# Kernel tuning notes

Hardware: AMD Instinct MI355X
Metric: run time of the kernel (lower is better)

Reference implementation:

```python
import jax, jax.numpy as jnp
from jax import lax
import numpy as np

CHANNEL_N = 16
EMB = 128
B, H, W = 16, 256, 256


def setup_inputs() -> dict:
    key = jax.random.key(0)
    ks = jax.random.split(key, 8)
    x = jax.random.uniform(ks[0], (B, CHANNEL_N, H, W), dtype=jnp.float32)
    fire_mask = (jax.random.uniform(ks[1], (B, 1, H, W)) < 0.5).astype(jnp.float32)
    s = 0.05
    w1 = jax.random.normal(ks[2], (3 * CHANNEL_N, EMB), dtype=jnp.float32) * s
    b1 = jnp.zeros((EMB,), jnp.float32)
    w2 = jax.random.normal(ks[3], (EMB, EMB), dtype=jnp.float32) * s
    b2 = jnp.zeros((EMB,), jnp.float32)
    w3 = jax.random.normal(ks[4], (EMB, CHANNEL_N), dtype=jnp.float32) * s
    b3 = jnp.zeros((CHANNEL_N,), jnp.float32)
    return {"x": x, "fire_mask": fire_mask, "w1": w1, "b1": b1, "w2": w2, "b2": b2, "w3": w3, "b3": b3}


def _forward(x, fire_mask, w1, b1, w2, b2, w3, b3):
    # depthwise Sobel conv (torch conv2d = cross-correlation, same as lax default)
    sob = jnp.array([[-1., 0., 1.], [-2., 0., 2.], [-1., 0., 1.]], jnp.float32)
    kx = jnp.tile(sob[None, None], (CHANNEL_N, 1, 1, 1))   # OIHW, groups=16
    ky = jnp.tile(sob.T[None, None], (CHANNEL_N, 1, 1, 1))
    conv = lambda k: lax.conv_general_dilated(x, k, (1, 1), 'SAME', feature_group_count=CHANNEL_N)
    feats = jnp.concatenate([x, conv(kx), conv(ky)], axis=1)  # [B,48,H,W]

    # alive mask: 3x3 max-pool of alpha channel > 0.1
    alpha = x[:, 3:4]
    pooled = lax.reduce_window(alpha, -jnp.inf, lax.max, (1, 1, 3, 3), (1, 1, 1, 1), 'SAME')
    alive = (pooled > 0.1).astype(x.dtype)
    combined = fire_mask * alive                     # [B,1,H,W]
    # nonzero-indexing semantics: update written wherever combined != 0
    sel = (combined != 0).astype(x.dtype)

    f = feats.transpose(0, 2, 3, 1)                  # [B,H,W,48]
    h = jax.nn.relu(f @ w1 + b1)
    h = jax.nn.relu(h @ w2 + b2)
    u = h @ w3 + b3                                  # [B,H,W,16]
    updates = u * sel.transpose(0, 2, 3, 1)          # zero outside selected cells
    return updates.transpose(0, 3, 1, 2)             # [B,16,H,W]


def reference(x, fire_mask, w1, b1, w2, b2, w3, b3):
    return _forward(x, fire_mask, w1, b1, w2, b2, w3, b3)
```

## Files before the change

kernel.cpp:

```cpp
#include <hip/hip_runtime.h>


using bf16x8 = __attribute__((ext_vector_type(8))) __bf16;
using f32x4  = __attribute__((ext_vector_type(4))) float;

__device__ __forceinline__ unsigned f2bf(float f) {
    unsigned u = __float_as_uint(f);
    u += 0x7fffu + ((u >> 16) & 1u);
    return u >> 16;
}

#define WS1_OFF 0
#define WS2_OFF 8192
#define WS3_OFF 24576

__global__ __launch_bounds__(256)
void prep_weights(const float* __restrict__ w1, const float* __restrict__ b1,
                  const float* __restrict__ w2, const float* __restrict__ w3,
                  unsigned short* __restrict__ ws) {
    const int gid = blockIdx.x * 256 + threadIdx.x;
    if (gid < 1024) {
        const int s = gid;
        const int mt = s >> 7, kb = (s >> 6) & 1, lane = s & 63;
        const int q = lane >> 4, ln = lane & 15;
#pragma unroll
        for (int j = 0; j < 8; ++j) {
            const int k = kb * 32 + q * 8 + j;
            float val = 0.f;
            if (k < 48) { const int c = k / 3, t = k - 3 * c; val = w1[(t * 16 + c) * 128 + mt * 16 + ln]; }
            else if (k == 48) val = b1[mt * 16 + ln];
            ws[WS1_OFF + s * 8 + j] = (unsigned short)f2bf(val);
        }
    } else if (gid < 3072) {
        const int s2 = gid - 1024;
        const int mt = s2 >> 8, kb = (s2 >> 6) & 3, lane = s2 & 63;
        const int q = lane >> 4, ln = lane & 15;
#pragma unroll
        for (int j = 0; j < 8; ++j) {
            const int k = kb * 32 + q * 8 + j;
            ws[WS2_OFF + s2 * 8 + j] = (unsigned short)f2bf(w2[k * 128 + mt * 16 + ln]);
        }
    } else if (gid < 3328) {
        const int s3 = gid - 3072;
        const int kb = s3 >> 6, lane = s3 & 63;
        const int q = lane >> 4, ln = lane & 15;
#pragma unroll
        for (int j = 0; j < 8; ++j) {
            const int k = kb * 32 + q * 8 + j;
            ws[WS3_OFF + s3 * 8 + j] = (unsigned short)f2bf(w3[k * 16 + ln]);
        }
    }
}


#define SM_XS    0
#define SM_W2    65536
#define SM_WR    98304
#define SM_AUX   155648
#define SM_B2L   159744
#define SM_B3L   160256
#define SM_TOTAL 160320

#define GLDS16(gp, lp) __builtin_amdgcn_global_load_lds(                     \
    (const __attribute__((address_space(1))) void*)(gp),                     \
    (__attribute__((address_space(3))) void*)(lp), 16, 0, 0)

#define STAGE_UNIT(chv, rowv) do {                                           \
        const int _sl = (rowv) & 3;                                          \
        char* _ld = smem + SM_XS + (size_t)(((_sl) * 16 + (chv)) * 256) * 4; \
        if ((unsigned)(rowv) < 256u) {                                       \
            const float* _gs = xb + ((size_t)(chv) << 16)                    \
                             + (size_t)(unsigned)(rowv) * 256 + lane * 4;    \
            GLDS16(_gs, _ld);                                                \
        } else {                                                             \
            *(float4*)(_ld + lane * 16) = make_float4(0.f, 0.f, 0.f, 0.f);   \
        } } while (0)

#define HCH(j) ((((j) ^ (ln & 7)) << 4))

extern "C" __global__ __launch_bounds__(512)
void fused_kernel(const float* __restrict__ x, const float* __restrict__ fmask,
                  const unsigned short* __restrict__ wf,
                  const float* __restrict__ b2, const float* __restrict__ b3,
                  float* __restrict__ out) {
    extern __shared__ char smem[];
    float (*xs)[16][256] = (float (*)[16][256])(smem + SM_XS);
    char* W2L = smem + SM_W2;

    const int t = threadIdx.x;
    const int wv = t >> 6, lane = t & 63;
    const int q = lane >> 4, ln = lane & 15;
    const int rhalf = t >> 8;
    const int col = t & 255;
    char* region = smem + SM_WR + wv * 7168;

    const int bb = blockIdx.x >> 5;
    const int h0 = (blockIdx.x & 31) << 3;
    const float* xb = x + ((size_t)bb << 20);

    {
        const uint4* s1 = (const uint4*)(wf + WS1_OFF);
        uint4* dW = (uint4*)W2L;
        dW[t]       = s1[t];
        dW[t + 512] = s1[t + 512];
        if (t < 256) ((uint4*)(smem + SM_AUX))[t] = ((const uint4*)(wf + WS3_OFF))[t];
        if (t < 128) ((float*)(smem + SM_B2L))[t] = b2[t];
        if (t < 16)  ((float*)(smem + SM_B3L))[t] = b3[t];
    }
    __syncthreads();
    bf16x8 W1f[8][2];
#pragma unroll
    for (int mt = 0; mt < 8; ++mt) {
        W1f[mt][0] = *(const bf16x8*)(W2L + ((mt * 2 + 0) * 64 + lane) * 16);
        W1f[mt][1] = *(const bf16x8*)(W2L + ((mt * 2 + 1) * 64 + lane) * 16);
    }
    __syncthreads();
    {
        const uint4* s2 = (const uint4*)(wf + WS2_OFF);
        uint4* dW = (uint4*)W2L;
#pragma unroll
        for (int i2 = 0; i2 < 4; ++i2) dW[t + i2 * 512] = s2[t + i2 * 512];
    }

    const int cL = (col > 0)   ? col - 1 : 0;
    const int cR = (col < 255) ? col + 1 : 255;
    const float mL = (col > 0)   ? 1.f : 0.f;
    const float mR = (col < 255) ? 1.f : 0.f;
    const int m7w = lane % 7;
    const int lq7 = ln % 7;

#pragma unroll
    for (int k = 0; k < 8; ++k) {
        const int u = wv + 8 * k;
        STAGE_UNIT(u >> 2, h0 - 1 + (u & 3));
    }

    for (int i = 0; i < 4; ++i) {
        const int r0 = h0 + 2 * i;
        const int r  = r0 + rhalf;
        __syncthreads();
        const float fv = fmask[((size_t)bb << 16) + (size_t)r * 256 + col];

        const int sT = (r - 1) & 3, sC = r & 3, sB = (r + 1) & 3;
        unsigned pk[24];
        unsigned carry = 0;
        float selv = 0.f;
#pragma unroll
        for (int c = 0; c < 16; ++c) {
            const float* rT = xs[sT][c];
            const float* rC = xs[sC][c];
            const float* rB = xs[sB][c];
            const float v00 = rT[cL] * mL, v01 = rT[col], v02 = rT[cR] * mR;
            const float v10 = rC[cL] * mL, v11 = rC[col], v12 = rC[cR] * mR;
            const float v20 = rB[cL] * mL, v21 = rB[col], v22 = rB[cR] * mR;
            const float sx = (v02 + 2.f * v12 + v22) - (v00 + 2.f * v10 + v20);
            const float sy = (v20 + 2.f * v21 + v22) - (v00 + 2.f * v01 + v02);
            if (c == 3) {
                float mx = fmaxf(fmaxf(fmaxf(v00, v01), fmaxf(v02, v10)),
                                 fmaxf(fmaxf(v11, v12), fmaxf(fmaxf(v20, v21), v22)));
                selv = (mx > 0.1f) ? 1.f : 0.f;
            }
            const unsigned ux = f2bf(v11), usx = f2bf(sx), usy = f2bf(sy);
            if ((c & 1) == 0) { pk[(c >> 1) * 3] = ux | (usx << 16); carry = usy; }
            else { pk[(c >> 1) * 3 + 1] = carry | (ux << 16);
                   pk[(c >> 1) * 3 + 2] = usx | (usy << 16); }
        }
        {
            char* fb = region + lane * 112;
#pragma unroll
            for (int c = 0; c < 6; ++c) {
                int pc = c + m7w; if (pc >= 7) pc -= 7;
                *(uint4*)(fb + pc * 16)
                    = make_uint4(pk[c * 4 + 0], pk[c * 4 + 1], pk[c * 4 + 2], pk[c * 4 + 3]);
            }
            const int pc6 = (m7w == 0) ? 6 : (m7w - 1);
            *(float*)(fb + pc6 * 16) = (fv != 0.f) ? selv : 0.f;
        }
        __syncthreads();
        if (i < 3) {
#pragma unroll
            for (int k = 0; k < 4; ++k) {
                const int u = wv + 8 * k;
                STAGE_UNIT(u >> 1, r0 + 3 + (u & 1));
            }
        }

#pragma unroll
        for (int p = 0; p < 2; ++p) {
            char* Hb = region + p * 3584;
            bf16x8 Bk0a[2], Bk1a[2];
            float sva[2];
#pragma unroll
            for (int s2 = 0; s2 < 2; ++s2) {
                const int s = p * 2 + s2;
                int v7 = 2 * s + lq7; if (v7 >= 7) v7 -= 7;
                const char* fp = region + (s * 16 + ln) * 112;
                int c0 = q + v7; if (c0 >= 7) c0 -= 7;
                Bk0a[s2] = *(const bf16x8*)(fp + c0 * 16);
                bf16x8 t1 = {};
                if (q < 2) { int c1 = 4 + q + v7; if (c1 >= 7) c1 -= 7;
                             t1 = *(const bf16x8*)(fp + c1 * 16); }
                else if (q == 2) t1[0] = (__bf16)1.0f;
                Bk1a[s2] = t1;
                const int c6 = (v7 == 0) ? 6 : (v7 - 1);
                sva[s2] = *(const float*)(fp + c6 * 16);
            }
            f32x4 a3h;
#pragma unroll
            for (int s2 = 0; s2 < 2; ++s2) {
                bf16x8 B2[4];
#pragma unroll
                for (int m = 0; m < 4; ++m) {
                    f32x4 a = {};
                    a = __builtin_amdgcn_mfma_f32_16x16x32_bf16(W1f[m][0], Bk0a[s2], a, 0, 0, 0);
                    a = __builtin_amdgcn_mfma_f32_16x16x32_bf16(W1f[m][1], Bk1a[s2], a, 0, 0, 0);
                    const unsigned r01 = f2bf(fmaxf(a[0], 0.f)) | (f2bf(fmaxf(a[1], 0.f)) << 16);
                    const unsigned r23 = f2bf(fmaxf(a[2], 0.f)) | (f2bf(fmaxf(a[3], 0.f)) << 16);
                    *(uint2*)(Hb + ln * 128 + HCH(m * 2 + (q >> 1)) + ((q & 1) << 3))
                        = make_uint2(r01, r23);
                }
                B2[0] = *(const bf16x8*)(Hb + ln * 128 + HCH(q));
                B2[1] = *(const bf16x8*)(Hb + ln * 128 + HCH(4 + q));
#pragma unroll
                for (int m = 4; m < 8; ++m) {
                    f32x4 a = {};
                    a = __builtin_amdgcn_mfma_f32_16x16x32_bf16(W1f[m][0], Bk0a[s2], a, 0, 0, 0);
                    a = __builtin_amdgcn_mfma_f32_16x16x32_bf16(W1f[m][1], Bk1a[s2], a, 0, 0, 0);
                    const unsigned r01 = f2bf(fmaxf(a[0], 0.f)) | (f2bf(fmaxf(a[1], 0.f)) << 16);
                    const unsigned r23 = f2bf(fmaxf(a[2], 0.f)) | (f2bf(fmaxf(a[3], 0.f)) << 16);
                    *(uint2*)(Hb + ln * 128 + HCH((m - 4) * 2 + (q >> 1)) + ((q & 1) << 3))
                        = make_uint2(r01, r23);
                }
                B2[2] = *(const bf16x8*)(Hb + ln * 128 + HCH(q));
                B2[3] = *(const bf16x8*)(Hb + ln * 128 + HCH(4 + q));
                bf16x8 B3[4];
#pragma unroll
                for (int m = 0; m < 4; ++m) {
                    f32x4 a = *(const f32x4*)(smem + SM_B2L + m * 64 + q * 16);
#pragma unroll
                    for (int kb = 0; kb < 4; ++kb) {
                        const bf16x8 Af = *(const bf16x8*)(W2L + ((m * 4 + kb) * 64 + lane) * 16);
                        a = __builtin_amdgcn_mfma_f32_16x16x32_bf16(Af, B2[kb], a, 0, 0, 0);
                    }
                    const unsigned r01 = f2bf(fmaxf(a[0], 0.f)) | (f2bf(fmaxf(a[1], 0.f)) << 16);
                    const unsigned r23 = f2bf(fmaxf(a[2], 0.f)) | (f2bf(fmaxf(a[3], 0.f)) << 16);
                    *(uint2*)(Hb + ln * 128 + HCH(m * 2 + (q >> 1)) + ((q & 1) << 3))
                        = make_uint2(r01, r23);
                }
                B3[0] = *(const bf16x8*)(Hb + ln * 128 + HCH(q));
                B3[1] = *(const bf16x8*)(Hb + ln * 128 + HCH(4 + q));
#pragma unroll
                for (int m = 4; m < 8; ++m) {
                    f32x4 a = *(const f32x4*)(smem + SM_B2L + m * 64 + q * 16);
#pragma unroll
                    for (int kb = 0; kb < 4; ++kb) {
                        const bf16x8 Af = *(const bf16x8*)(W2L + ((m * 4 + kb) * 64 + lane) * 16);
                        a = __builtin_amdgcn_mfma_f32_16x16x32_bf16(Af, B2[kb], a, 0, 0, 0);
                    }
                    const unsigned r01 = f2bf(fmaxf(a[0], 0.f)) | (f2bf(fmaxf(a[1], 0.f)) << 16);
                    const unsigned r23 = f2bf(fmaxf(a[2], 0.f)) | (f2bf(fmaxf(a[3], 0.f)) << 16);
                    *(uint2*)(Hb + ln * 128 + HCH((m - 4) * 2 + (q >> 1)) + ((q & 1) << 3))
                        = make_uint2(r01, r23);
                }
                B3[2] = *(const bf16x8*)(Hb + ln * 128 + HCH(q));
                B3[3] = *(const bf16x8*)(Hb + ln * 128 + HCH(4 + q));
                f32x4 a3 = *(const f32x4*)(smem + SM_B3L + q * 16);
#pragma unroll
                for (int kb = 0; kb < 4; ++kb) {
                    const bf16x8 W3a = *(const bf16x8*)(smem + SM_AUX + (kb * 64 + lane) * 16);
                    a3 = __builtin_amdgcn_mfma_f32_16x16x32_bf16(W3a, B3[kb], a3, 0, 0, 0);
                }
                const float svv = sva[s2];
#pragma unroll
                for (int r4 = 0; r4 < 4; ++r4) a3[r4] *= svv;
                if (s2 == 0) a3h = a3;
                else {
#pragma unroll
                    for (int r4 = 0; r4 < 4; ++r4) {
                        *(float*)(Hb + (q * 4 + r4) * 132 + ln * 4)      = a3h[r4];
                        *(float*)(Hb + (q * 4 + r4) * 132 + 64 + ln * 4) = a3[r4];
                    }
                }
            }
        }
        {
            float* orow = out + (((size_t)(bb * 16)) << 16) + (size_t)r * 256
                        + (wv & 3) * 64 + lane;
#pragma unroll
            for (int ch = 0; ch < 16; ++ch) {
                const float v = *(const float*)(region + (lane >> 5) * 3584
                              + ch * 132 + ((lane >> 4) & 1) * 64 + (lane & 15) * 4);
                orow[(size_t)ch << 16] = v;
            }
        }
    }
}

extern "C" void kernel_launch(void* const* d_in, const int* in_sizes, int n_in,
                              void* d_out, int out_size, void* d_ws, size_t ws_size,
                              hipStream_t stream) {
    (void)in_sizes; (void)n_in; (void)out_size; (void)ws_size;
    const float* x  = (const float*)d_in[0];
    const float* fm = (const float*)d_in[1];
    const float* w1 = (const float*)d_in[2];
    const float* b1 = (const float*)d_in[3];
    const float* w2 = (const float*)d_in[4];
    const float* b2 = (const float*)d_in[5];
    const float* w3 = (const float*)d_in[6];
    const float* b3 = (const float*)d_in[7];
    float* o = (float*)d_out;
    unsigned short* ws = (unsigned short*)d_ws;

    prep_weights<<<dim3(13), dim3(256), 0, stream>>>(w1, b1, w2, w3, ws);

    hipFuncSetAttribute((const void*)fused_kernel,
                        hipFuncAttributeMaxDynamicSharedMemorySize, SM_TOTAL);
    fused_kernel<<<dim3(512), dim3(512), SM_TOTAL, stream>>>(x, fm, ws, b2, b3, o);
}
```

Measured before the change: 259.5 us.

## Drop rotated LDS feature layout, interleave stores, add MFMA priority hints

Replaces the per-lane rotated (mod 7) LDS layout of packed features with a fixed layout. Each 16-byte chunk is written as soon as its channels are packed, which cuts index arithmetic and lets the pk registers die early. Wraps MFMA blocks in s_setprio raises so waves in the matrix phase get issue priority, and caches the hipFuncSetAttribute call on the host. The fixed layout may bring back LDS bank conflicts on the row-strided reads and writes that the rotation was meant to avoid.

```diff
diff --git a/kernel.cpp b/kernel.cpp
--- a/kernel.cpp
+++ b/kernel.cpp
@@ -126,8 +126,6 @@
     const int cR = (col < 255) ? col + 1 : 255;
     const float mL = (col > 0)   ? 1.f : 0.f;
     const float mR = (col < 255) ? 1.f : 0.f;
-    const int m7w = lane % 7;
-    const int lq7 = ln % 7;
 
 #pragma unroll
     for (int k = 0; k < 8; ++k) {
@@ -142,9 +140,9 @@
         const float fv = fmask[((size_t)bb << 16) + (size_t)r * 256 + col];
 
         const int sT = (r - 1) & 3, sC = r & 3, sB = (r + 1) & 3;
+        char* fb = region + lane * 112;
         unsigned pk[24];
         unsigned carry = 0;
-        float selv = 0.f;
 #pragma unroll
         for (int c = 0; c < 16; ++c) {
             const float* rT = xs[sT][c];
@@ -158,23 +156,19 @@
             if (c == 3) {
                 float mx = fmaxf(fmaxf(fmaxf(v00, v01), fmaxf(v02, v10)),
                                  fmaxf(fmaxf(v11, v12), fmaxf(fmaxf(v20, v21), v22)));
-                selv = (mx > 0.1f) ? 1.f : 0.f;
+                const float selv = (mx > 0.1f) ? 1.f : 0.f;
+                *(float*)(fb + 96) = (fv != 0.f) ? selv : 0.f;
             }
             const unsigned ux = f2bf(v11), usx = f2bf(sx), usy = f2bf(sy);
             if ((c & 1) == 0) { pk[(c >> 1) * 3] = ux | (usx << 16); carry = usy; }
             else { pk[(c >> 1) * 3 + 1] = carry | (ux << 16);
                    pk[(c >> 1) * 3 + 2] = usx | (usy << 16); }
-        }
-        {
-            char* fb = region + lane * 112;
-#pragma unroll
-            for (int c = 0; c < 6; ++c) {
-                int pc = c + m7w; if (pc >= 7) pc -= 7;
-                *(uint4*)(fb + pc * 16)
-                    = make_uint4(pk[c * 4 + 0], pk[c * 4 + 1], pk[c * 4 + 2], pk[c * 4 + 3]);
-            }
-            const int pc6 = (m7w == 0) ? 6 : (m7w - 1);
-            *(float*)(fb + pc6 * 16) = (fv != 0.f) ? selv : 0.f;
+            if (c == 2)  *(uint4*)(fb +  0) = make_uint4(pk[0],  pk[1],  pk[2],  pk[3]);
+            if (c == 5)  *(uint4*)(fb + 16) = make_uint4(pk[4],  pk[5],  pk[6],  pk[7]);
+            if (c == 8)  *(uint4*)(fb + 32) = make_uint4(pk[8],  pk[9],  pk[10], pk[11]);
+            if (c == 10) *(uint4*)(fb + 48) = make_uint4(pk[12], pk[13], pk[14], pk[15]);
+            if (c == 13) *(uint4*)(fb + 64) = make_uint4(pk[16], pk[17], pk[18], pk[19]);
+            if (c == 15) *(uint4*)(fb + 80) = make_uint4(pk[20], pk[21], pk[22], pk[23]);
         }
         __syncthreads();
         if (i < 3) {
@@ -193,22 +187,19 @@
 #pragma unroll
             for (int s2 = 0; s2 < 2; ++s2) {
                 const int s = p * 2 + s2;
-                int v7 = 2 * s + lq7; if (v7 >= 7) v7 -= 7;
                 const char* fp = region + (s * 16 + ln) * 112;
-                int c0 = q + v7; if (c0 >= 7) c0 -= 7;
-                Bk0a[s2] = *(const bf16x8*)(fp + c0 * 16);
+                Bk0a[s2] = *(const bf16x8*)(fp + q * 16);
                 bf16x8 t1 = {};
-                if (q < 2) { int c1 = 4 + q + v7; if (c1 >= 7) c1 -= 7;
-                             t1 = *(const bf16x8*)(fp + c1 * 16); }
+                if (q < 2)       t1 = *(const bf16x8*)(fp + (4 + q) * 16);
                 else if (q == 2) t1[0] = (__bf16)1.0f;
                 Bk1a[s2] = t1;
-                const int c6 = (v7 == 0) ? 6 : (v7 - 1);
-                sva[s2] = *(const float*)(fp + c6 * 16);
+                sva[s2] = *(const float*)(fp + 96);
             }
             f32x4 a3h;
 #pragma unroll
             for (int s2 = 0; s2 < 2; ++s2) {
                 bf16x8 B2[4];
+                __builtin_amdgcn_s_setprio(1);
 #pragma unroll
                 for (int m = 0; m < 4; ++m) {
                     f32x4 a = {};
@@ -219,8 +210,10 @@
                     *(uint2*)(Hb + ln * 128 + HCH(m * 2 + (q >> 1)) + ((q & 1) << 3))
                         = make_uint2(r01, r23);
                 }
+                __builtin_amdgcn_s_setprio(0);
                 B2[0] = *(const bf16x8*)(Hb + ln * 128 + HCH(q));
                 B2[1] = *(const bf16x8*)(Hb + ln * 128 + HCH(4 + q));
+                __builtin_amdgcn_s_setprio(1);
 #pragma unroll
                 for (int m = 4; m < 8; ++m) {
                     f32x4 a = {};
@@ -231,9 +224,11 @@
                     *(uint2*)(Hb + ln * 128 + HCH((m - 4) * 2 + (q >> 1)) + ((q & 1) << 3))
                         = make_uint2(r01, r23);
                 }
+                __builtin_amdgcn_s_setprio(0);
                 B2[2] = *(const bf16x8*)(Hb + ln * 128 + HCH(q));
                 B2[3] = *(const bf16x8*)(Hb + ln * 128 + HCH(4 + q));
                 bf16x8 B3[4];
+                __builtin_amdgcn_s_setprio(1);
 #pragma unroll
                 for (int m = 0; m < 4; ++m) {
                     f32x4 a = *(const f32x4*)(smem + SM_B2L + m * 64 + q * 16);
@@ -247,8 +242,10 @@
                     *(uint2*)(Hb + ln * 128 + HCH(m * 2 + (q >> 1)) + ((q & 1) << 3))
                         = make_uint2(r01, r23);
                 }
+                __builtin_amdgcn_s_setprio(0);
                 B3[0] = *(const bf16x8*)(Hb + ln * 128 + HCH(q));
                 B3[1] = *(const bf16x8*)(Hb + ln * 128 + HCH(4 + q));
+                __builtin_amdgcn_s_setprio(1);
 #pragma unroll
                 for (int m = 4; m < 8; ++m) {
                     f32x4 a = *(const f32x4*)(smem + SM_B2L + m * 64 + q * 16);
@@ -262,14 +259,17 @@
                     *(uint2*)(Hb + ln * 128 + HCH((m - 4) * 2 + (q >> 1)) + ((q & 1) << 3))
                         = make_uint2(r01, r23);
                 }
+                __builtin_amdgcn_s_setprio(0);
                 B3[2] = *(const bf16x8*)(Hb + ln * 128 + HCH(q));
                 B3[3] = *(const bf16x8*)(Hb + ln * 128 + HCH(4 + q));
                 f32x4 a3 = *(const f32x4*)(smem + SM_B3L + q * 16);
+                __builtin_amdgcn_s_setprio(1);
 #pragma unroll
                 for (int kb = 0; kb < 4; ++kb) {
                     const bf16x8 W3a = *(const bf16x8*)(smem + SM_AUX + (kb * 64 + lane) * 16);
                     a3 = __builtin_amdgcn_mfma_f32_16x16x32_bf16(W3a, B3[kb], a3, 0, 0, 0);
                 }
+                __builtin_amdgcn_s_setprio(0);
                 const float svv = sva[s2];
 #pragma unroll
                 for (int r4 = 0; r4 < 4; ++r4) a3[r4] *= svv;
@@ -313,7 +313,11 @@
 
     prep_weights<<<dim3(13), dim3(256), 0, stream>>>(w1, b1, w2, w3, ws);
 
-    hipFuncSetAttribute((const void*)fused_kernel,
-                        hipFuncAttributeMaxDynamicSharedMemorySize, SM_TOTAL);
+    static bool s_attr_done = false;
+    if (!s_attr_done) {
+        hipFuncSetAttribute((const void*)fused_kernel,
+                            hipFuncAttributeMaxDynamicSharedMemorySize, SM_TOTAL);
+        s_attr_done = true;
+    }
     fused_kernel<<<dim3(512), dim3(512), SM_TOTAL, stream>>>(x, fm, ws, b2, b3, o);
 }
```

Result: faster. 220.9 us (-14.9%).
